# Kernel optimization log

Hardware: AMD Instinct MI355X
Metric: run time of the kernel (lower is better)

## Reference

```python
import jax, jax.numpy as jnp
import numpy as np
from jax import lax

EMBED = 768
D_INNER = 2 * EMBED          # expand = 2
D_STATE = 16
D_CONV = 4
DT_RANK = (EMBED + 15) // 16  # 48
FF = 3072
B, L = 2, 1024


def setup_inputs() -> dict:
    key = jax.random.key(0)
    ks = jax.random.split(key, 20)
    s = 0.02
    inp = {
        "x": jax.random.normal(ks[0], (B, L, EMBED), jnp.float32),
        # Mamba params
        "in_proj_w": jax.random.normal(ks[1], (2 * D_INNER, EMBED), jnp.float32) * s,
        "conv_w": jax.random.normal(ks[2], (D_INNER, 1, D_CONV), jnp.float32) * s,
        "conv_b": jnp.zeros((D_INNER,), jnp.float32),
        "x_proj_w": jax.random.normal(ks[3], (DT_RANK + 2 * D_STATE, D_INNER), jnp.float32) * s,
        "dt_proj_w": jax.random.normal(ks[4], (D_INNER, DT_RANK), jnp.float32) * s,
        "dt_proj_b": jax.random.normal(ks[5], (D_INNER,), jnp.float32) * s,
        "A_log": jnp.log(jnp.broadcast_to(jnp.arange(1, D_STATE + 1, dtype=jnp.float32), (D_INNER, D_STATE))),
        "D_param": jnp.ones((D_INNER,), jnp.float32),
        "out_proj_w": jax.random.normal(ks[6], (EMBED, D_INNER), jnp.float32) * s,
        # block params
        "ln1_w": jnp.ones((EMBED,), jnp.float32), "ln1_b": jnp.zeros((EMBED,), jnp.float32),
        "ln2_w": jnp.ones((EMBED,), jnp.float32), "ln2_b": jnp.zeros((EMBED,), jnp.float32),
        "ffn_w1": jax.random.normal(ks[7], (FF, EMBED), jnp.float32) * s,
        "ffn_b1": jnp.zeros((FF,), jnp.float32),
        "ffn_w2": jax.random.normal(ks[8], (EMBED, FF), jnp.float32) * s,
        "ffn_b2": jnp.zeros((EMBED,), jnp.float32),
    }
    return inp


def _layernorm(x, w, b, eps=1e-5):
    mu = jnp.mean(x, -1, keepdims=True)
    var = jnp.mean((x - mu) ** 2, -1, keepdims=True)
    return (x - mu) * lax.rsqrt(var + eps) * w + b


def _mamba(x, in_proj_w, conv_w, conv_b, x_proj_w, dt_proj_w, dt_proj_b,
           A_log, D_param, out_proj_w):
    # x: [B, L, E]
    xz = jnp.einsum('ble,de->bld', x, in_proj_w)          # [B,L,2*Di]
    xin, z = jnp.split(xz, 2, axis=-1)                    # [B,L,Di] each
    # causal depthwise conv over time
    xc = lax.conv_general_dilated(
        xin.transpose(0, 2, 1), conv_w, window_strides=(1,),
        padding=[(D_CONV - 1, 0)], feature_group_count=D_INNER,
        dimension_numbers=('NCH', 'OIH', 'NCH'))
    xc = (xc + conv_b[None, :, None]).transpose(0, 2, 1)  # [B,L,Di]
    xc = jax.nn.silu(xc)
    # input-dependent SSM params
    x_dbl = jnp.einsum('bld,rd->blr', xc, x_proj_w)       # [B,L,dt_rank+2n]
    dt, Bm, Cm = jnp.split(x_dbl, [DT_RANK, DT_RANK + D_STATE], axis=-1)
    delta = jax.nn.softplus(jnp.einsum('blr,dr->bld', dt, dt_proj_w) + dt_proj_b)
    A = -jnp.exp(A_log)                                   # [Di, n]
    deltaA = jnp.exp(jnp.einsum('bld,dn->bldn', delta, A))
    deltaBu = jnp.einsum('bld,bln,bld->bldn', delta, Bm, xc)

    def step(h, xs):
        dA, dBu, Ct = xs                                  # [B,Di,n],[B,Di,n],[B,n]
        h = dA * h + dBu
        y = jnp.einsum('bdn,bn->bd', h, Ct)
        return h, y

    h0 = jnp.zeros((x.shape[0], D_INNER, D_STATE), x.dtype)
    _, ys = lax.scan(step, h0, (deltaA.transpose(1, 0, 2, 3),
                                deltaBu.transpose(1, 0, 2, 3),
                                Cm.transpose(1, 0, 2)))
    y = ys.transpose(1, 0, 2)                             # [B,L,Di]
    y = y + xc * D_param
    y = y * jax.nn.silu(z)
    return jnp.einsum('bld,ed->ble', y, out_proj_w)


def reference(x, in_proj_w, conv_w, conv_b, x_proj_w, dt_proj_w, dt_proj_b,
              A_log, D_param, out_proj_w, ln1_w, ln1_b, ln2_w, ln2_b,
              ffn_w1, ffn_b1, ffn_w2, ffn_b2):
    # dropout is identity in eval mode
    h = _mamba(x, in_proj_w, conv_w, conv_b, x_proj_w, dt_proj_w, dt_proj_b,
               A_log, D_param, out_proj_w)
    x1 = _layernorm(h + x, ln1_w, ln1_b)
    f = jnp.einsum('ble,fe->blf', x1, ffn_w1) + ffn_b1
    f = jax.nn.gelu(f)
    f = jnp.einsum('blf,ef->ble', f, ffn_w2) + ffn_b2
    return _layernorm(f + x1, ln2_w, ln2_b)
```

## Files before the change

kernel.cpp:

```cpp
#include <hip/hip_runtime.h>
#include <math.h>

#define EMBED 768
#define DI 1536
#define DSTATE 16
#define DCONV 4
#define DTRANK 48
#define FF 3072
#define BATCH 2
#define SEQ 1024
#define NROWS (BATCH*SEQ)
#define TCH 32
#define NCH (SEQ/TCH)
#define DBLK 64

typedef __bf16 bf16x8 __attribute__((ext_vector_type(8)));
typedef float f32x4 __attribute__((ext_vector_type(4)));
typedef unsigned int u32x4 __attribute__((ext_vector_type(4)));

static __device__ __forceinline__ unsigned short f2b(float f) {
    union { float f; unsigned u; } v; v.f = f;
    unsigned r = v.u + 0x7FFFu + ((v.u >> 16) & 1u);
    return (unsigned short)(r >> 16);
}
static __device__ __forceinline__ float b2f(unsigned short s) {
    union { unsigned u; float f; } v; v.u = ((unsigned)s) << 16;
    return v.f;
}

#define GLOAD_LDS16(g, l) __builtin_amdgcn_global_load_lds( \
    (const __attribute__((address_space(1))) void*)(g), \
    (__attribute__((address_space(3))) void*)(l), 16, 0, 0)

template<int EPI, int KSPLIT>
__global__ __launch_bounds__(256)
void gemm_sk(const unsigned short* __restrict__ A,
             const unsigned short* __restrict__ W,
             float* __restrict__ C, unsigned short* __restrict__ Cb,
             float* __restrict__ part,
             int M, int N, int K,
             const float* __restrict__ bias)
{
    __shared__ alignas(16) unsigned short As[2][128 * 32];
    __shared__ alignas(16) unsigned short Ws[2][64 * 32];
    const int tid  = threadIdx.x;
    const int lane = tid & 63, wave = tid >> 6;
    const int bm = blockIdx.y * 128, bn = blockIdx.x * 64;
    const int kc = K / KSPLIT;
    const int kz = blockIdx.z * kc;
    const int ln = lane & 15, lg = lane >> 4;

    f32x4 acc[2][4];
    #pragma unroll
    for (int i = 0; i < 2; ++i)
        #pragma unroll
        for (int j = 0; j < 4; ++j)
            acc[i][j] = (f32x4){0.f, 0.f, 0.f, 0.f};

    const int ra = tid >> 2, ca = tid & 3;
    const int cs = (ca * 8) ^ ((ra & 3) << 3);
    const unsigned short* gA0 = A + (size_t)(bm + ra) * K + kz + cs;
    const unsigned short* gA1 = A + (size_t)(bm + ra + 64) * K + kz + cs;
    const unsigned short* gW  = W + (size_t)(bn + ra) * K + kz + cs;

#define STAGE(bf, kk) do { \
        GLOAD_LDS16(gA0 + (kk), &As[bf][wave * 512]); \
        GLOAD_LDS16(gA1 + (kk), &As[bf][2048 + wave * 512]); \
        GLOAD_LDS16(gW  + (kk), &Ws[bf][wave * 512]); \
    } while (0)

    STAGE(0, 0);
    __syncthreads();
    int buf = 0;
    for (int k0 = 0; k0 < kc; k0 += 32) {
        if (k0 + 32 < kc) STAGE(buf ^ 1, k0 + 32);
        bf16x8 af[2], wf[4];
        #pragma unroll
        for (int i = 0; i < 2; ++i) {
            int row = wave * 32 + i * 16 + ln;
            af[i] = *reinterpret_cast<const bf16x8*>(
                &As[buf][row * 32 + ((lg * 8) ^ ((row & 3) << 3))]);
        }
        #pragma unroll
        for (int j = 0; j < 4; ++j) {
            int row = j * 16 + ln;
            wf[j] = *reinterpret_cast<const bf16x8*>(
                &Ws[buf][row * 32 + ((lg * 8) ^ ((row & 3) << 3))]);
        }
        #pragma unroll
        for (int i = 0; i < 2; ++i)
            #pragma unroll
            for (int j = 0; j < 4; ++j)
                acc[i][j] = __builtin_amdgcn_mfma_f32_16x16x32_bf16(af[i], wf[j], acc[i][j], 0, 0, 0);
        __syncthreads();
        buf ^= 1;
    }
#undef STAGE

    if constexpr (KSPLIT > 1) {
        float* pb = part + (size_t)blockIdx.z * M * N;
        #pragma unroll
        for (int i = 0; i < 2; ++i)
            #pragma unroll
            for (int j = 0; j < 4; ++j) {
                int col = bn + j * 16 + ln;
                #pragma unroll
                for (int rr = 0; rr < 4; ++rr) {
                    int row = bm + wave * 32 + i * 16 + lg * 4 + rr;
                    pb[(size_t)row * N + col] = acc[i][j][rr];
                }
            }
    } else {
        #pragma unroll
        for (int i = 0; i < 2; ++i)
            #pragma unroll
            for (int j = 0; j < 4; ++j) {
                int col = bn + j * 16 + ln;
                #pragma unroll
                for (int rr = 0; rr < 4; ++rr) {
                    int row = bm + wave * 32 + i * 16 + lg * 4 + rr;
                    float v = acc[i][j][rr];
                    size_t o = (size_t)row * N + col;
                    if (EPI == 1) {
                        v += bias[col];
                        C[o] = (v > 20.f) ? v : log1pf(expf(v));
                    } else if (EPI == 3) {
                        v += bias[col];
                        float t = 0.7978845608028654f * (v + 0.044715f * v * v * v);
                        Cb[o] = f2b(0.5f * v * (1.f + tanhf(t)));
                    } else if (EPI == 6) {
                        Cb[o] = f2b(v);
                    } else {
                        C[o] = v;
                    }
                }
            }
    }
}

template<int KS, int BIAS>
__global__ __launch_bounds__(256)
void reduce_ln(const float* __restrict__ part, const float* __restrict__ resid,
               const float* __restrict__ bias,
               const float* __restrict__ w, const float* __restrict__ bb,
               float* __restrict__ out, unsigned short* __restrict__ outb)
{
    const int row = blockIdx.x;
    const size_t ro = (size_t)row * EMBED;
    const int i0 = threadIdx.x, i1 = i0 + 256, i2 = i0 + 512;
    float v0 = 0.f, v1 = 0.f, v2 = 0.f;
    #pragma unroll
    for (int z = 0; z < KS; ++z) {
        const float* p = part + (size_t)z * NROWS * EMBED + ro;
        v0 += p[i0]; v1 += p[i1]; v2 += p[i2];
    }
    if (BIAS) { v0 += bias[i0]; v1 += bias[i1]; v2 += bias[i2]; }
    v0 += resid[ro + i0]; v1 += resid[ro + i1]; v2 += resid[ro + i2];

    float s  = v0 + v1 + v2;
    float s2 = v0 * v0 + v1 * v1 + v2 * v2;
    #pragma unroll
    for (int m = 1; m < 64; m <<= 1) {
        s  += __shfl_xor(s,  m);
        s2 += __shfl_xor(s2, m);
    }
    __shared__ float sh1[4], sh2[4];
    int wv = threadIdx.x >> 6;
    if ((threadIdx.x & 63) == 0) { sh1[wv] = s; sh2[wv] = s2; }
    __syncthreads();
    float S1 = sh1[0] + sh1[1] + sh1[2] + sh1[3];
    float S2 = sh2[0] + sh2[1] + sh2[2] + sh2[3];
    float mu  = S1 * (1.f / EMBED);
    float var = S2 * (1.f / EMBED) - mu * mu;
    float rs  = rsqrtf(var + 1e-5f);
    float o0 = (v0 - mu) * rs * w[i0] + bb[i0];
    float o1 = (v1 - mu) * rs * w[i1] + bb[i1];
    float o2 = (v2 - mu) * rs * w[i2] + bb[i2];
    out[ro + i0] = o0; out[ro + i1] = o1; out[ro + i2] = o2;
    if (outb) {
        outb[ro + i0] = f2b(o0); outb[ro + i1] = f2b(o1); outb[ro + i2] = f2b(o2);
    }
}

__global__ __launch_bounds__(256)
void xproj_mfma(const unsigned short* __restrict__ A,
                const unsigned short* __restrict__ W,
                float* __restrict__ part)
{
    const int mt = blockIdx.x, s = blockIdx.y;
    const int lane = threadIdx.x & 63, wave = threadIdx.x >> 6;
    const int ln = lane & 15, lg = lane >> 4;
    const int row0 = mt * 128 + wave * 32;
    const int kb = s * 192;
    f32x4 acc[2][5];
    #pragma unroll
    for (int i = 0; i < 2; ++i)
        #pragma unroll
        for (int j = 0; j < 5; ++j)
            acc[i][j] = (f32x4){0.f, 0.f, 0.f, 0.f};

    for (int kk = 0; kk < 192; kk += 32) {
        const int k = kb + kk + lg * 8;
        bf16x8 af[2], wf[5];
        af[0] = *reinterpret_cast<const bf16x8*>(A + (size_t)(row0 + ln) * DI + k);
        af[1] = *reinterpret_cast<const bf16x8*>(A + (size_t)(row0 + 16 + ln) * DI + k);
        #pragma unroll
        for (int j = 0; j < 5; ++j)
            wf[j] = *reinterpret_cast<const bf16x8*>(W + (size_t)(j * 16 + ln) * DI + k);
        #pragma unroll
        for (int i = 0; i < 2; ++i)
            #pragma unroll
            for (int j = 0; j < 5; ++j)
                acc[i][j] = __builtin_amdgcn_mfma_f32_16x16x32_bf16(af[i], wf[j], acc[i][j], 0, 0, 0);
    }
    float* pb = part + (size_t)s * NROWS * 80;
    #pragma unroll
    for (int i = 0; i < 2; ++i)
        #pragma unroll
        for (int j = 0; j < 5; ++j)
            #pragma unroll
            for (int rr = 0; rr < 4; ++rr) {
                int row = row0 + i * 16 + lg * 4 + rr;
                int col = j * 16 + ln;
                pb[(size_t)row * 80 + col] = acc[i][j][rr];
            }
}

__global__ __launch_bounds__(256)
void xproj_reduce(const float* __restrict__ part, float* __restrict__ xdbl,
                  unsigned short* __restrict__ xdblb)
{
    int idx = blockIdx.x * 256 + threadIdx.x;
    float sum = 0.f;
    #pragma unroll
    for (int s = 0; s < 8; ++s) sum += part[(size_t)s * NROWS * 80 + idx];
    xdbl[idx] = sum;
    int col = idx % 80, row = idx / 80;
    if (col < 48)      xdblb[row * 64 + col] = f2b(sum);
    else if (col < 64) xdblb[row * 64 + col] = 0;
}

__global__ __launch_bounds__(256)
void cvt7_k(const float* __restrict__ x,  const float* __restrict__ w1,
            const float* __restrict__ w2, const float* __restrict__ w3,
            const float* __restrict__ w4, const float* __restrict__ w5,
            const float* __restrict__ w6,
            unsigned short* __restrict__ xb,  unsigned short* __restrict__ w1b,
            unsigned short* __restrict__ w2b, unsigned short* __restrict__ w3b,
            unsigned short* __restrict__ w4b, unsigned short* __restrict__ w5b,
            unsigned short* __restrict__ w6b)
{
    size_t i4 = ((size_t)blockIdx.x * 256 + threadIdx.x) * 4;
    if (i4 >= 9953280u) {
        int off = (int)(i4 - 9953280u);
        if (off >= 98304) return;
        int row = off >> 6, colb = off & 63;
        ushort4 u = {0, 0, 0, 0};
        if (colb < 48) {
            float4 v = *reinterpret_cast<const float4*>(w6 + row * 48 + colb);
            u.x = f2b(v.x); u.y = f2b(v.y); u.z = f2b(v.z); u.w = f2b(v.w);
        }
        *reinterpret_cast<ushort4*>(w6b + off) = u;
        return;
    }
    const float* src; unsigned short* dst; size_t off;
    if      (i4 < 1572864u) { src = x;  dst = xb;  off = i4; }
    else if (i4 < 3932160u) { src = w1; dst = w1b; off = i4 - 1572864u; }
    else if (i4 < 5111808u) { src = w2; dst = w2b; off = i4 - 3932160u; }
    else if (i4 < 7471104u) { src = w3; dst = w3b; off = i4 - 5111808u; }
    else if (i4 < 9830400u) { src = w4; dst = w4b; off = i4 - 7471104u; }
    else                    { src = w5; dst = w5b; off = i4 - 9830400u; }
    float4 v = *reinterpret_cast<const float4*>(src + off);
    ushort4 u;
    u.x = f2b(v.x); u.y = f2b(v.y); u.z = f2b(v.z); u.w = f2b(v.w);
    *reinterpret_cast<ushort4*>(dst + off) = u;
}

__global__ __launch_bounds__(256)
void conv_silu_k(const unsigned short* __restrict__ xz, const float* __restrict__ cw,
                 const float* __restrict__ cb, float* __restrict__ xc,
                 unsigned short* __restrict__ xcb)
{
    int q = blockIdx.x * 256 + threadIdx.x;
    int d4 = (q * 4) % DI;
    int bt = (q * 4) / DI;
    int t  = bt % SEQ;
    const unsigned short* base = xz + (size_t)bt * (2 * DI) + d4;
    float4 acc = *reinterpret_cast<const float4*>(cb + d4);
    float4 wv0 = *reinterpret_cast<const float4*>(cw + (d4 + 0) * 4);
    float4 wv1 = *reinterpret_cast<const float4*>(cw + (d4 + 1) * 4);
    float4 wv2 = *reinterpret_cast<const float4*>(cw + (d4 + 2) * 4);
    float4 wv3 = *reinterpret_cast<const float4*>(cw + (d4 + 3) * 4);
    {
        ushort4 r = *reinterpret_cast<const ushort4*>(base);
        acc.x += wv0.w * b2f(r.x); acc.y += wv1.w * b2f(r.y);
        acc.z += wv2.w * b2f(r.z); acc.w += wv3.w * b2f(r.w);
    }
    if (t >= 1) {
        ushort4 r = *reinterpret_cast<const ushort4*>(base - 2 * DI);
        acc.x += wv0.z * b2f(r.x); acc.y += wv1.z * b2f(r.y);
        acc.z += wv2.z * b2f(r.z); acc.w += wv3.z * b2f(r.w);
    }
    if (t >= 2) {
        ushort4 r = *reinterpret_cast<const ushort4*>(base - 4 * DI);
        acc.x += wv0.y * b2f(r.x); acc.y += wv1.y * b2f(r.y);
        acc.z += wv2.y * b2f(r.z); acc.w += wv3.y * b2f(r.w);
    }
    if (t >= 3) {
        ushort4 r = *reinterpret_cast<const ushort4*>(base - 6 * DI);
        acc.x += wv0.x * b2f(r.x); acc.y += wv1.x * b2f(r.y);
        acc.z += wv2.x * b2f(r.z); acc.w += wv3.x * b2f(r.w);
    }
    float4 v;
    v.x = acc.x / (1.f + __expf(-acc.x));
    v.y = acc.y / (1.f + __expf(-acc.y));
    v.z = acc.z / (1.f + __expf(-acc.z));
    v.w = acc.w / (1.f + __expf(-acc.w));
    size_t o = (size_t)bt * DI + d4;
    *reinterpret_cast<float4*>(xc + o) = v;
    ushort4 u; u.x = f2b(v.x); u.y = f2b(v.y); u.z = f2b(v.z); u.w = f2b(v.w);
    *reinterpret_cast<ushort4*>(xcb + o) = u;
}

__global__ __launch_bounds__(256)
void scan2_a(const float* __restrict__ delta, const float* __restrict__ xc,
             const float* __restrict__ xdbl,  const float* __restrict__ A_log,
             float* __restrict__ hfin, float* __restrict__ aprod)
{
    const int d0 = blockIdx.x * DBLK, ch = blockIdx.y, b = blockIdx.z;
    const int t0 = ch * TCH;
    __shared__ float del_s[TCH][DBLK + 4];
    __shared__ float xc_s[TCH][DBLK + 4];
    __shared__ float b_s[TCH][20];
    const int tid = threadIdx.x;
    {
        const int c4 = tid & 15, tr = tid >> 4;
        #pragma unroll
        for (int p = 0; p < 2; ++p) {
            int t = p * 16 + tr;
            size_t rowo = (size_t)(b * SEQ + t0 + t);
            *reinterpret_cast<float4*>(&del_s[t][c4 * 4]) =
                *reinterpret_cast<const float4*>(&delta[rowo * DI + d0 + c4 * 4]);
            *reinterpret_cast<float4*>(&xc_s[t][c4 * 4]) =
                *reinterpret_cast<const float4*>(&xc[rowo * DI + d0 + c4 * 4]);
        }
        const int cbq = tid & 3, tb = tid >> 2;
        if (tb < TCH) {
            size_t rowo = (size_t)(b * SEQ + t0 + tb);
            *reinterpret_cast<float4*>(&b_s[tb][cbq * 4]) =
                *reinterpret_cast<const float4*>(&xdbl[rowo * 80 + DTRANK + cbq * 4]);
        }
    }
    __syncthreads();
    const int lane = tid & 63, wave = tid >> 6;
    const int wd = wave * 16 + (lane >> 2);
    const int d = d0 + wd;
    const int nq = (lane & 3) * 4;
    float4 Av = *reinterpret_cast<const float4*>(&A_log[d * DSTATE + nq]);
    const float A0 = -__expf(Av.x), A1 = -__expf(Av.y), A2 = -__expf(Av.z), A3 = -__expf(Av.w);
    float h0_ = 0.f, h1_ = 0.f, h2_ = 0.f, h3_ = 0.f;
    float p0 = 1.f, p1 = 1.f, p2 = 1.f, p3 = 1.f;
    #pragma unroll 4
    for (int t = 0; t < TCH; ++t) {
        float dl = del_s[t][wd];
        float u  = dl * xc_s[t][wd];
        float4 bq = *reinterpret_cast<const float4*>(&b_s[t][nq]);
        float e0 = __expf(dl * A0), e1 = __expf(dl * A1);
        float e2 = __expf(dl * A2), e3 = __expf(dl * A3);
        h0_ = e0 * h0_ + u * bq.x; p0 *= e0;
        h1_ = e1 * h1_ + u * bq.y; p1 *= e1;
        h2_ = e2 * h2_ + u * bq.z; p2 *= e2;
        h3_ = e3 * h3_ + u * bq.w; p3 *= e3;
    }
    size_t o = ((size_t)((b * NCH + ch) * DI) + d) * DSTATE + nq;
    *reinterpret_cast<float4*>(&hfin[o])  = (float4){h0_, h1_, h2_, h3_};
    *reinterpret_cast<float4*>(&aprod[o]) = (float4){p0, p1, p2, p3};
}

__global__ __launch_bounds__(256)
void scan2_b(const float* __restrict__ hfin, const float* __restrict__ aprod,
             float* __restrict__ h0)
{
    int idx = blockIdx.x * 256 + threadIdx.x;
    int nq = (idx & 3) * 4;
    int d  = (idx >> 2) % DI;
    int b  = (idx >> 2) / DI;
    float4 h = {0.f, 0.f, 0.f, 0.f};
    #pragma unroll
    for (int ch = 0; ch < NCH; ++ch) {
        size_t o = ((size_t)((b * NCH + ch) * DI) + d) * DSTATE + nq;
        *reinterpret_cast<float4*>(&h0[o]) = h;
        float4 a = *reinterpret_cast<const float4*>(&aprod[o]);
        float4 f = *reinterpret_cast<const float4*>(&hfin[o]);
        h.x = a.x * h.x + f.x; h.y = a.y * h.y + f.y;
        h.z = a.z * h.z + f.z; h.w = a.w * h.w + f.w;
    }
}

__global__ __launch_bounds__(256)
void scan2_c(const float* __restrict__ delta, const float* __restrict__ xc,
             const float* __restrict__ xdbl,  const float* __restrict__ A_log,
             const float* __restrict__ Dp,    const unsigned short* __restrict__ xz,
             const float* __restrict__ h0,
             unsigned short* __restrict__ yb)
{
    const int d0 = blockIdx.x * DBLK, ch = blockIdx.y, b = blockIdx.z;
    const int t0 = ch * TCH;
    __shared__ float del_s[TCH][DBLK + 4];
    __shared__ float xc_s[TCH][DBLK + 4];
    __shared__ float b_s[TCH][20];
    __shared__ float c_s[TCH][20];
    __shared__ unsigned short z_s[TCH][DBLK + 8];
    const int tid = threadIdx.x;
    {
        const int c4 = tid & 15, tr = tid >> 4;
        #pragma unroll
        for (int p = 0; p < 2; ++p) {
            int t = p * 16 + tr;
            size_t rowo = (size_t)(b * SEQ + t0 + t);
            *reinterpret_cast<float4*>(&del_s[t][c4 * 4]) =
                *reinterpret_cast<const float4*>(&delta[rowo * DI + d0 + c4 * 4]);
            *reinterpret_cast<float4*>(&xc_s[t][c4 * 4]) =
                *reinterpret_cast<const float4*>(&xc[rowo * DI + d0 + c4 * 4]);
        }
        const int cbq = tid & 3, tb = tid >> 2;
        if (tb < TCH) {
            size_t rowo = (size_t)(b * SEQ + t0 + tb);
            *reinterpret_cast<float4*>(&b_s[tb][cbq * 4]) =
                *reinterpret_cast<const float4*>(&xdbl[rowo * 80 + DTRANK + cbq * 4]);
        } else {
            size_t rowo = (size_t)(b * SEQ + t0 + tb - TCH);
            *reinterpret_cast<float4*>(&c_s[tb - TCH][cbq * 4]) =
                *reinterpret_cast<const float4*>(&xdbl[rowo * 80 + DTRANK + DSTATE + cbq * 4]);
        }
        const int cz = tid & 7, tz = tid >> 3;
        size_t rz = (size_t)(b * SEQ + t0 + tz);
        *reinterpret_cast<u32x4*>(&z_s[tz][cz * 8]) =
            *reinterpret_cast<const u32x4*>(&xz[rz * (2 * DI) + DI + d0 + cz * 8]);
    }
    __syncthreads();
    const int lane = tid & 63, wave = tid >> 6;
    const int wd = wave * 16 + (lane >> 2);
    const int d = d0 + wd;
    const int nq = (lane & 3) * 4;
    float4 Av = *reinterpret_cast<const float4*>(&A_log[d * DSTATE + nq]);
    const float A0 = -__expf(Av.x), A1 = -__expf(Av.y), A2 = -__expf(Av.z), A3 = -__expf(Av.w);
    const float Dd = Dp[d];
    float4 h = *reinterpret_cast<const float4*>(
        &h0[((size_t)((b * NCH + ch) * DI) + d) * DSTATE + nq]);
    unsigned short* yrow = yb + (size_t)(b * SEQ + t0) * DI + d;
    #pragma unroll 4
    for (int t = 0; t < TCH; ++t) {
        float dl = del_s[t][wd];
        float xv = xc_s[t][wd];
        float u  = dl * xv;
        float4 bq = *reinterpret_cast<const float4*>(&b_s[t][nq]);
        float4 cq = *reinterpret_cast<const float4*>(&c_s[t][nq]);
        float e0 = __expf(dl * A0), e1 = __expf(dl * A1);
        float e2 = __expf(dl * A2), e3 = __expf(dl * A3);
        h.x = e0 * h.x + u * bq.x;
        h.y = e1 * h.y + u * bq.y;
        h.z = e2 * h.z + u * bq.z;
        h.w = e3 * h.w + u * bq.w;
        float py = h.x * cq.x + h.y * cq.y + h.z * cq.z + h.w * cq.w;
        py += __shfl_xor(py, 1);
        py += __shfl_xor(py, 2);
        if ((lane & 3) == 0) {
            float yv = py + xv * Dd;
            float zv = b2f(z_s[t][wd]);
            yv *= zv / (1.f + __expf(-zv));
            yrow[(size_t)t * DI] = f2b(yv);
        }
    }
}

extern "C" void kernel_launch(void* const* d_in, const int* in_sizes, int n_in,
                              void* d_out, int out_size, void* d_ws, size_t ws_size,
                              hipStream_t stream)
{
    const float* x         = (const float*)d_in[0];
    const float* in_proj_w = (const float*)d_in[1];
    const float* conv_w    = (const float*)d_in[2];
    const float* conv_b    = (const float*)d_in[3];
    const float* x_proj_w  = (const float*)d_in[4];
    const float* dt_proj_w = (const float*)d_in[5];
    const float* dt_proj_b = (const float*)d_in[6];
    const float* A_log     = (const float*)d_in[7];
    const float* D_param   = (const float*)d_in[8];
    const float* out_proj_w= (const float*)d_in[9];
    const float* ln1_w     = (const float*)d_in[10];
    const float* ln1_b     = (const float*)d_in[11];
    const float* ln2_w     = (const float*)d_in[12];
    const float* ln2_b     = (const float*)d_in[13];
    const float* ffn_w1    = (const float*)d_in[14];
    const float* ffn_b1    = (const float*)d_in[15];
    const float* ffn_w2    = (const float*)d_in[16];
    const float* ffn_b2    = (const float*)d_in[17];
    float* out = (float*)d_out;

    char* Wp = (char*)d_ws;
    #define MB(n) ((size_t)(n) * 1048576)
    unsigned short* xzb   = (unsigned short*)(Wp + 0);
    float*          xc    = (float*)         (Wp + MB(16));
    unsigned short* xcb   = (unsigned short*)(Wp + MB(30));
    float*          xdbl  = (float*)         (Wp + MB(38));
    unsigned short* xdblb = (unsigned short*)(Wp + MB(40));
    float*          delta = (float*)         (Wp + MB(42));
    unsigned short* ybb   = (unsigned short*)(Wp + MB(56));
    float*          hfin  = (float*)         (Wp + MB(66));
    float*          aprod = (float*)         (Wp + MB(76));
    float*          h0    = (float*)         (Wp + MB(86));
    unsigned short* xb    = (unsigned short*)(Wp + MB(92));
    unsigned short* wib   = (unsigned short*)(Wp + MB(96));
    unsigned short* wob   = (unsigned short*)(Wp + MB(101));
    unsigned short* wf1b  = (unsigned short*)(Wp + MB(104));
    unsigned short* wf2b  = (unsigned short*)(Wp + MB(109));
    unsigned short* xpwb  = (unsigned short*)(Wp + MB(114));
    unsigned short* wdtb  = (unsigned short*)(Wp + MB(115));
    float*          part  = (float*)         (Wp + MB(116));
    float*          part_op = (float*)       (Wp + MB(122));
    float*          part_f2 = (float*)       (Wp + MB(148));
    float*          x1    = (float*)         (Wp + MB(174));
    unsigned short* x1b   = (unsigned short*)(Wp + MB(181));
    unsigned short* fbf   = (unsigned short*)(Wp + MB(185));
    #undef MB

    dim3 blk(256);

    cvt7_k<<<9816, blk, 0, stream>>>(x, in_proj_w, out_proj_w, ffn_w1, ffn_w2, x_proj_w,
                                     dt_proj_w, xb, wib, wob, wf1b, wf2b, xpwb, wdtb);

    gemm_sk<6, 1><<<dim3(48, 16, 1), blk, 0, stream>>>(xb, wib, nullptr, xzb, nullptr,
                                                       NROWS, 2 * DI, EMBED, nullptr);

    conv_silu_k<<<(BATCH * SEQ * DI) / 1024, blk, 0, stream>>>(xzb, conv_w, conv_b, xc, xcb);

    xproj_mfma<<<dim3(16, 8), blk, 0, stream>>>(xcb, xpwb, part);
    xproj_reduce<<<640, blk, 0, stream>>>(part, xdbl, xdblb);

    gemm_sk<1, 1><<<dim3(24, 16, 1), blk, 0, stream>>>(xdblb, wdtb, delta, nullptr, nullptr,
                                                       NROWS, DI, 64, dt_proj_b);

    scan2_a<<<dim3(DI / DBLK, NCH, BATCH), blk, 0, stream>>>(delta, xc, xdbl, A_log, hfin, aprod);
    scan2_b<<<48, blk, 0, stream>>>(hfin, aprod, h0);
    scan2_c<<<dim3(DI / DBLK, NCH, BATCH), blk, 0, stream>>>(delta, xc, xdbl, A_log, D_param,
                                                             xzb, h0, ybb);

    gemm_sk<0, 4><<<dim3(12, 16, 4), blk, 0, stream>>>(ybb, wob, nullptr, nullptr, part_op,
                                                       NROWS, EMBED, DI, nullptr);
    reduce_ln<4, 0><<<NROWS, blk, 0, stream>>>(part_op, x, nullptr, ln1_w, ln1_b, x1, x1b);

    gemm_sk<3, 1><<<dim3(48, 16, 1), blk, 0, stream>>>(x1b, wf1b, nullptr, fbf, nullptr,
                                                       NROWS, FF, EMBED, ffn_b1);

    gemm_sk<0, 4><<<dim3(12, 16, 4), blk, 0, stream>>>(fbf, wf2b, nullptr, nullptr, part_f2,
                                                       NROWS, EMBED, FF, nullptr);
    reduce_ln<4, 1><<<NROWS, blk, 0, stream>>>(part_f2, x1, ffn_b2, ln2_w, ln2_b, out, nullptr);
}
```

Baseline: 205.5 us.

## Drop fp32 conv output and fold chunk-carry scan into scan2_c

The conv kernel now writes only the bf16 copy of the SiLU output. Both scan kernels read that bf16 copy instead of an fp32 tensor, which halves that traffic and removes one 12MB write. The separate scan2_b kernel that propagated chunk carries is removed. Each scan2_c block now recomputes its initial state by looping over all preceding chunks' hfin/aprod, with that loop overlapping the shared-memory loads before the barrier. This saves a launch and the h0 buffer, but adds redundant per-block work that grows with the chunk index and uses bf16-rounded x in the scan and skip term, which lowers precision.

```diff
diff --git a/kernel.cpp b/kernel.cpp
--- a/kernel.cpp
+++ b/kernel.cpp
@@ -278,8 +278,7 @@
 
 __global__ __launch_bounds__(256)
 void conv_silu_k(const unsigned short* __restrict__ xz, const float* __restrict__ cw,
-                 const float* __restrict__ cb, float* __restrict__ xc,
-                 unsigned short* __restrict__ xcb)
+                 const float* __restrict__ cb, unsigned short* __restrict__ xcb)
 {
     int q = blockIdx.x * 256 + threadIdx.x;
     int d4 = (q * 4) % DI;
@@ -311,26 +310,23 @@
         acc.x += wv0.x * b2f(r.x); acc.y += wv1.x * b2f(r.y);
         acc.z += wv2.x * b2f(r.z); acc.w += wv3.x * b2f(r.w);
     }
-    float4 v;
-    v.x = acc.x / (1.f + __expf(-acc.x));
-    v.y = acc.y / (1.f + __expf(-acc.y));
-    v.z = acc.z / (1.f + __expf(-acc.z));
-    v.w = acc.w / (1.f + __expf(-acc.w));
-    size_t o = (size_t)bt * DI + d4;
-    *reinterpret_cast<float4*>(xc + o) = v;
-    ushort4 u; u.x = f2b(v.x); u.y = f2b(v.y); u.z = f2b(v.z); u.w = f2b(v.w);
-    *reinterpret_cast<ushort4*>(xcb + o) = u;
-}
-
-__global__ __launch_bounds__(256)
-void scan2_a(const float* __restrict__ delta, const float* __restrict__ xc,
+    ushort4 u;
+    u.x = f2b(acc.x / (1.f + __expf(-acc.x)));
+    u.y = f2b(acc.y / (1.f + __expf(-acc.y)));
+    u.z = f2b(acc.z / (1.f + __expf(-acc.z)));
+    u.w = f2b(acc.w / (1.f + __expf(-acc.w)));
+    *reinterpret_cast<ushort4*>(xcb + (size_t)bt * DI + d4) = u;
+}
+
+__global__ __launch_bounds__(256)
+void scan2_a(const float* __restrict__ delta, const unsigned short* __restrict__ xcb,
              const float* __restrict__ xdbl,  const float* __restrict__ A_log,
              float* __restrict__ hfin, float* __restrict__ aprod)
 {
     const int d0 = blockIdx.x * DBLK, ch = blockIdx.y, b = blockIdx.z;
     const int t0 = ch * TCH;
     __shared__ float del_s[TCH][DBLK + 4];
-    __shared__ float xc_s[TCH][DBLK + 4];
+    __shared__ unsigned short xc_s[TCH][DBLK + 8];
     __shared__ float b_s[TCH][20];
     const int tid = threadIdx.x;
     {
@@ -341,9 +337,11 @@
             size_t rowo = (size_t)(b * SEQ + t0 + t);
             *reinterpret_cast<float4*>(&del_s[t][c4 * 4]) =
                 *reinterpret_cast<const float4*>(&delta[rowo * DI + d0 + c4 * 4]);
-            *reinterpret_cast<float4*>(&xc_s[t][c4 * 4]) =
-                *reinterpret_cast<const float4*>(&xc[rowo * DI + d0 + c4 * 4]);
-        }
+        }
+        const int cz = tid & 7, tz = tid >> 3;
+        size_t rz = (size_t)(b * SEQ + t0 + tz);
+        *reinterpret_cast<u32x4*>(&xc_s[tz][cz * 8]) =
+            *reinterpret_cast<const u32x4*>(&xcb[rz * DI + d0 + cz * 8]);
         const int cbq = tid & 3, tb = tid >> 2;
         if (tb < TCH) {
             size_t rowo = (size_t)(b * SEQ + t0 + tb);
@@ -363,7 +361,7 @@
     #pragma unroll 4
     for (int t = 0; t < TCH; ++t) {
         float dl = del_s[t][wd];
-        float u  = dl * xc_s[t][wd];
+        float u  = dl * b2f(xc_s[t][wd]);
         float4 bq = *reinterpret_cast<const float4*>(&b_s[t][nq]);
         float e0 = __expf(dl * A0), e1 = __expf(dl * A1);
         float e2 = __expf(dl * A2), e3 = __expf(dl * A3);
@@ -378,36 +376,16 @@
 }
 
 __global__ __launch_bounds__(256)
-void scan2_b(const float* __restrict__ hfin, const float* __restrict__ aprod,
-             float* __restrict__ h0)
-{
-    int idx = blockIdx.x * 256 + threadIdx.x;
-    int nq = (idx & 3) * 4;
-    int d  = (idx >> 2) % DI;
-    int b  = (idx >> 2) / DI;
-    float4 h = {0.f, 0.f, 0.f, 0.f};
-    #pragma unroll
-    for (int ch = 0; ch < NCH; ++ch) {
-        size_t o = ((size_t)((b * NCH + ch) * DI) + d) * DSTATE + nq;
-        *reinterpret_cast<float4*>(&h0[o]) = h;
-        float4 a = *reinterpret_cast<const float4*>(&aprod[o]);
-        float4 f = *reinterpret_cast<const float4*>(&hfin[o]);
-        h.x = a.x * h.x + f.x; h.y = a.y * h.y + f.y;
-        h.z = a.z * h.z + f.z; h.w = a.w * h.w + f.w;
-    }
-}
-
-__global__ __launch_bounds__(256)
-void scan2_c(const float* __restrict__ delta, const float* __restrict__ xc,
+void scan2_c(const float* __restrict__ delta, const unsigned short* __restrict__ xcb,
              const float* __restrict__ xdbl,  const float* __restrict__ A_log,
              const float* __restrict__ Dp,    const unsigned short* __restrict__ xz,
-             const float* __restrict__ h0,
+             const float* __restrict__ hfin,  const float* __restrict__ aprod,
              unsigned short* __restrict__ yb)
 {
     const int d0 = blockIdx.x * DBLK, ch = blockIdx.y, b = blockIdx.z;
     const int t0 = ch * TCH;
     __shared__ float del_s[TCH][DBLK + 4];
-    __shared__ float xc_s[TCH][DBLK + 4];
+    __shared__ unsigned short xc_s[TCH][DBLK + 8];
     __shared__ float b_s[TCH][20];
     __shared__ float c_s[TCH][20];
     __shared__ unsigned short z_s[TCH][DBLK + 8];
@@ -420,9 +398,13 @@
             size_t rowo = (size_t)(b * SEQ + t0 + t);
             *reinterpret_cast<float4*>(&del_s[t][c4 * 4]) =
                 *reinterpret_cast<const float4*>(&delta[rowo * DI + d0 + c4 * 4]);
-            *reinterpret_cast<float4*>(&xc_s[t][c4 * 4]) =
-                *reinterpret_cast<const float4*>(&xc[rowo * DI + d0 + c4 * 4]);
-        }
+        }
+        const int cz = tid & 7, tz = tid >> 3;
+        size_t rz = (size_t)(b * SEQ + t0 + tz);
+        *reinterpret_cast<u32x4*>(&xc_s[tz][cz * 8]) =
+            *reinterpret_cast<const u32x4*>(&xcb[rz * DI + d0 + cz * 8]);
+        *reinterpret_cast<u32x4*>(&z_s[tz][cz * 8]) =
+            *reinterpret_cast<const u32x4*>(&xz[rz * (2 * DI) + DI + d0 + cz * 8]);
         const int cbq = tid & 3, tb = tid >> 2;
         if (tb < TCH) {
             size_t rowo = (size_t)(b * SEQ + t0 + tb);
@@ -433,26 +415,30 @@
             *reinterpret_cast<float4*>(&c_s[tb - TCH][cbq * 4]) =
                 *reinterpret_cast<const float4*>(&xdbl[rowo * 80 + DTRANK + DSTATE + cbq * 4]);
         }
-        const int cz = tid & 7, tz = tid >> 3;
-        size_t rz = (size_t)(b * SEQ + t0 + tz);
-        *reinterpret_cast<u32x4*>(&z_s[tz][cz * 8]) =
-            *reinterpret_cast<const u32x4*>(&xz[rz * (2 * DI) + DI + d0 + cz * 8]);
-    }
-    __syncthreads();
+    }
     const int lane = tid & 63, wave = tid >> 6;
     const int wd = wave * 16 + (lane >> 2);
     const int d = d0 + wd;
     const int nq = (lane & 3) * 4;
+
+    float4 h = {0.f, 0.f, 0.f, 0.f};
+    for (int cc = 0; cc < ch; ++cc) {
+        size_t o = ((size_t)((b * NCH + cc) * DI) + d) * DSTATE + nq;
+        float4 a = *reinterpret_cast<const float4*>(&aprod[o]);
+        float4 f = *reinterpret_cast<const float4*>(&hfin[o]);
+        h.x = a.x * h.x + f.x; h.y = a.y * h.y + f.y;
+        h.z = a.z * h.z + f.z; h.w = a.w * h.w + f.w;
+    }
+
     float4 Av = *reinterpret_cast<const float4*>(&A_log[d * DSTATE + nq]);
     const float A0 = -__expf(Av.x), A1 = -__expf(Av.y), A2 = -__expf(Av.z), A3 = -__expf(Av.w);
     const float Dd = Dp[d];
-    float4 h = *reinterpret_cast<const float4*>(
-        &h0[((size_t)((b * NCH + ch) * DI) + d) * DSTATE + nq]);
+    __syncthreads();
     unsigned short* yrow = yb + (size_t)(b * SEQ + t0) * DI + d;
     #pragma unroll 4
     for (int t = 0; t < TCH; ++t) {
         float dl = del_s[t][wd];
-        float xv = xc_s[t][wd];
+        float xv = b2f(xc_s[t][wd]);
         float u  = dl * xv;
         float4 bq = *reinterpret_cast<const float4*>(&b_s[t][nq]);
         float4 cq = *reinterpret_cast<const float4*>(&c_s[t][nq]);
@@ -501,28 +487,26 @@
     char* Wp = (char*)d_ws;
     #define MB(n) ((size_t)(n) * 1048576)
     unsigned short* xzb   = (unsigned short*)(Wp + 0);
-    float*          xc    = (float*)         (Wp + MB(16));
-    unsigned short* xcb   = (unsigned short*)(Wp + MB(30));
-    float*          xdbl  = (float*)         (Wp + MB(38));
-    unsigned short* xdblb = (unsigned short*)(Wp + MB(40));
-    float*          delta = (float*)         (Wp + MB(42));
-    unsigned short* ybb   = (unsigned short*)(Wp + MB(56));
-    float*          hfin  = (float*)         (Wp + MB(66));
-    float*          aprod = (float*)         (Wp + MB(76));
-    float*          h0    = (float*)         (Wp + MB(86));
-    unsigned short* xb    = (unsigned short*)(Wp + MB(92));
-    unsigned short* wib   = (unsigned short*)(Wp + MB(96));
-    unsigned short* wob   = (unsigned short*)(Wp + MB(101));
-    unsigned short* wf1b  = (unsigned short*)(Wp + MB(104));
-    unsigned short* wf2b  = (unsigned short*)(Wp + MB(109));
-    unsigned short* xpwb  = (unsigned short*)(Wp + MB(114));
-    unsigned short* wdtb  = (unsigned short*)(Wp + MB(115));
-    float*          part  = (float*)         (Wp + MB(116));
-    float*          part_op = (float*)       (Wp + MB(122));
-    float*          part_f2 = (float*)       (Wp + MB(148));
-    float*          x1    = (float*)         (Wp + MB(174));
-    unsigned short* x1b   = (unsigned short*)(Wp + MB(181));
-    unsigned short* fbf   = (unsigned short*)(Wp + MB(185));
+    unsigned short* xcb   = (unsigned short*)(Wp + MB(16));
+    float*          xdbl  = (float*)         (Wp + MB(24));
+    unsigned short* xdblb = (unsigned short*)(Wp + MB(26));
+    float*          delta = (float*)         (Wp + MB(28));
+    unsigned short* ybb   = (unsigned short*)(Wp + MB(42));
+    float*          hfin  = (float*)         (Wp + MB(50));
+    float*          aprod = (float*)         (Wp + MB(58));
+    unsigned short* xb    = (unsigned short*)(Wp + MB(66));
+    unsigned short* wib   = (unsigned short*)(Wp + MB(70));
+    unsigned short* wob   = (unsigned short*)(Wp + MB(75));
+    unsigned short* wf1b  = (unsigned short*)(Wp + MB(78));
+    unsigned short* wf2b  = (unsigned short*)(Wp + MB(83));
+    unsigned short* xpwb  = (unsigned short*)(Wp + MB(88));
+    unsigned short* wdtb  = (unsigned short*)(Wp + MB(89));
+    float*          part  = (float*)         (Wp + MB(90));
+    float*          part_op = (float*)       (Wp + MB(96));
+    float*          part_f2 = (float*)       (Wp + MB(122));
+    float*          x1    = (float*)         (Wp + MB(148));
+    unsigned short* x1b   = (unsigned short*)(Wp + MB(155));
+    unsigned short* fbf   = (unsigned short*)(Wp + MB(159));
     #undef MB
 
     dim3 blk(256);
@@ -533,7 +517,7 @@
     gemm_sk<6, 1><<<dim3(48, 16, 1), blk, 0, stream>>>(xb, wib, nullptr, xzb, nullptr,
                                                        NROWS, 2 * DI, EMBED, nullptr);
 
-    conv_silu_k<<<(BATCH * SEQ * DI) / 1024, blk, 0, stream>>>(xzb, conv_w, conv_b, xc, xcb);
+    conv_silu_k<<<(BATCH * SEQ * DI) / 1024, blk, 0, stream>>>(xzb, conv_w, conv_b, xcb);
 
     xproj_mfma<<<dim3(16, 8), blk, 0, stream>>>(xcb, xpwb, part);
     xproj_reduce<<<640, blk, 0, stream>>>(part, xdbl, xdblb);
@@ -541,10 +525,9 @@
     gemm_sk<1, 1><<<dim3(24, 16, 1), blk, 0, stream>>>(xdblb, wdtb, delta, nullptr, nullptr,
                                                        NROWS, DI, 64, dt_proj_b);
 
-    scan2_a<<<dim3(DI / DBLK, NCH, BATCH), blk, 0, stream>>>(delta, xc, xdbl, A_log, hfin, aprod);
-    scan2_b<<<48, blk, 0, stream>>>(hfin, aprod, h0);
-    scan2_c<<<dim3(DI / DBLK, NCH, BATCH), blk, 0, stream>>>(delta, xc, xdbl, A_log, D_param,
-                                                             xzb, h0, ybb);
+    scan2_a<<<dim3(DI / DBLK, NCH, BATCH), blk, 0, stream>>>(delta, xcb, xdbl, A_log, hfin, aprod);
+    scan2_c<<<dim3(DI / DBLK, NCH, BATCH), blk, 0, stream>>>(delta, xcb, xdbl, A_log, D_param,
+                                                             xzb, hfin, aprod, ybb);
 
     gemm_sk<0, 4><<<dim3(12, 16, 4), blk, 0, stream>>>(ybb, wob, nullptr, nullptr, part_op,
                                                        NROWS, EMBED, DI, nullptr);
```

New measurement: 201.5 us. Within noise of the previous version (-1.9%).
